# Kernel optimization log

Hardware: AMD Instinct MI355X
Metric: run time of the kernel (lower is better)

## Reference

```python
import jax, jax.numpy as jnp
import numpy as np
import math

N_HEADS = 16
HEAD_DIM = 64
D_MODEL = 1024
B, S = 2, 2048


def setup_inputs() -> dict:
    key = jax.random.key(0)
    ks = jax.random.split(key, 12)
    Dh = N_HEADS * HEAD_DIM
    sc = 1.0 / math.sqrt(D_MODEL)
    return {
        "will_be_queries": jax.random.normal(ks[0], (B, S, D_MODEL), jnp.float32),
        "will_be_keys": jax.random.normal(ks[1], (B, S, D_MODEL), jnp.float32),
        "will_be_values": jax.random.normal(ks[2], (B, S, D_MODEL), jnp.float32),
        "valid_len": jax.random.randint(ks[3], (B,), 1, S + 1, jnp.int32),
        # torch nn.Linear weights: (out_features, in_features)
        "w_q": jax.random.normal(ks[4], (Dh, D_MODEL), jnp.float32) * sc,
        "b_q": jnp.zeros((Dh,), jnp.float32),
        "w_k": jax.random.normal(ks[5], (Dh, D_MODEL), jnp.float32) * sc,
        "b_k": jnp.zeros((Dh,), jnp.float32),
        "w_v": jax.random.normal(ks[6], (Dh, D_MODEL), jnp.float32) * sc,
        "b_v": jnp.zeros((Dh,), jnp.float32),
        "w_o": jax.random.normal(ks[7], (D_MODEL, Dh), jnp.float32) * sc,
        "b_o": jnp.zeros((D_MODEL,), jnp.float32),
    }


def _split_heads(x):
    # (B, S, H*Dh) -> (B, H, S, Dh)
    b, s, _ = x.shape
    return x.reshape(b, s, N_HEADS, HEAD_DIM).transpose(0, 2, 1, 3)


def reference(will_be_queries, will_be_keys, will_be_values, valid_len,
              w_q, b_q, w_k, b_k, w_v, b_v, w_o, b_o):
    q = _split_heads(will_be_queries @ w_q.T + b_q)   # (B,H,S,Dh)
    k = _split_heads(will_be_keys @ w_k.T + b_k)
    v = _split_heads(will_be_values @ w_v.T + b_v)

    scores = jnp.einsum("bhqd,bhkd->bhqk", q, k) / jnp.sqrt(
        jnp.asarray(HEAD_DIM, q.dtype))

    neg = jnp.finfo(scores.dtype).min
    q_idx = jnp.arange(scores.shape[2])[:, None]   # (S,1)
    k_idx = jnp.arange(scores.shape[3])[None, :]   # (1,S)
    causal = k_idx > q_idx                         # look-ahead mask (offset=1 triu)
    vmask = k_idx[None] >= valid_len[:, None, None]  # (B,S,S) keys beyond valid_len
    mask = causal[None, None] | vmask[:, None]       # (B,1|H,S,S) broadcast over heads
    scores = jnp.where(mask, neg, scores)

    attn = jax.nn.softmax(scores, axis=-1)
    out = jnp.einsum("bhqk,bhkd->bhqd", attn, v)   # (B,H,S,Dh)
    out = out.transpose(0, 2, 1, 3).reshape(out.shape[0], out.shape[2], N_HEADS * HEAD_DIM)
    return out @ w_o.T + b_o
```

## Files before the change

kernel.cpp:

```cpp
#include <hip/hip_runtime.h>
#include <math.h>

#define NH 16
#define HD 64
#define DM 1024
#define BB 2
#define SS 2048
#define MROWS (BB*SS)
#define MEG 1048576

typedef __attribute__((ext_vector_type(8))) short bf16x8;
typedef __attribute__((ext_vector_type(4))) float f32x4;

__device__ __forceinline__ unsigned short f2bf(float x) {
    unsigned int u = __float_as_uint(x);
    u += 0x7fff + ((u >> 16) & 1);
    return (unsigned short)(u >> 16);
}

__device__ __forceinline__ unsigned int pack2bf(float a, float b) {
    return (unsigned int)f2bf(a) | ((unsigned int)f2bf(b) << 16);
}

#define GLD_LDS16(gp, lp) __builtin_amdgcn_global_load_lds(                  \
        (const __attribute__((address_space(1))) void*)(gp),                 \
        (__attribute__((address_space(3))) void*)(lp), 16, 0, 0)

__global__ __launch_bounds__(256)
void cvt_all(const float* __restrict__ xq, const float* __restrict__ xk,
             const float* __restrict__ xv, const float* __restrict__ wq,
             const float* __restrict__ wk, const float* __restrict__ wv,
             const float* __restrict__ wo, unsigned short* __restrict__ ws)
{
    const int reg = blockIdx.y;
    const size_t n    = (reg < 3) ? (size_t)4 * MEG : (size_t)MEG;
    const size_t roff = (reg < 3) ? (size_t)reg * 4 * MEG
                                  : (size_t)12 * MEG + (size_t)(reg - 3) * MEG;
    const float* src = (reg == 0) ? xq : (reg == 1) ? xk : (reg == 2) ? xv :
                       (reg == 3) ? wq : (reg == 4) ? wk : (reg == 5) ? wv : wo;
    const size_t i = ((size_t)blockIdx.x * 256 + threadIdx.x) * 8;
    if (i >= n) return;
    const float4 a = *(const float4*)(src + i);
    const float4 b = *(const float4*)(src + i + 4);
    ushort4 lo4, hi4;
    lo4.x = f2bf(a.x); lo4.y = f2bf(a.y); lo4.z = f2bf(a.z); lo4.w = f2bf(a.w);
    hi4.x = f2bf(b.x); hi4.y = f2bf(b.y); hi4.z = f2bf(b.z); hi4.w = f2bf(b.w);
    *(ushort4*)(ws + roff + i)     = lo4;
    *(ushort4*)(ws + roff + i + 4) = hi4;
}

template<int MODE>
__device__ __forceinline__ void gemm_mfma_core(
    const unsigned short* __restrict__ A,
    const unsigned short* __restrict__ W,
    const float* __restrict__ bias,
    void* __restrict__ Y, int ldy,
    unsigned short* __restrict__ As,
    unsigned short* __restrict__ Bs)
{
    const int tid  = threadIdx.x;
    const int w    = tid >> 6;
    const int lane = tid & 63;
    const int lo   = lane & 15;
    const int g    = lane >> 4;
    const int wr   = (w >> 1) * 64;
    const int wc   = (w & 1) * 64;

    f32x4 acc[4][4];
#pragma unroll
    for (int i = 0; i < 4; ++i)
#pragma unroll
        for (int j = 0; j < 4; ++j) acc[i][j] = (f32x4)0.f;

    for (int k0 = 0; k0 < 1024; k0 += 64) {
        __syncthreads();
#pragma unroll
        for (int u = 0; u < 4; ++u) {
            const int ci  = u * 256 + tid;
            const int row = ci >> 3, c = ci & 7;
            const int sc  = (c ^ (row & 7)) * 8;
            GLD_LDS16(A + (size_t)row * 1024 + k0 + sc, As + ci * 8);
            GLD_LDS16(W + (size_t)row * 1024 + k0 + sc, Bs + ci * 8);
        }
        asm volatile("s_waitcnt vmcnt(0)" ::: "memory");
        __syncthreads();

#pragma unroll
        for (int kk = 0; kk < 2; ++kk) {
            bf16x8 af[4], bf[4];
#pragma unroll
            for (int i = 0; i < 4; ++i) {
                const int ra = wr + i * 16 + lo;
                const int rb = wc + i * 16 + lo;
                af[i] = *(const bf16x8*)(As + ra * 64 + (((kk * 4 + g) ^ (ra & 7)) * 8));
                bf[i] = *(const bf16x8*)(Bs + rb * 64 + (((kk * 4 + g) ^ (rb & 7)) * 8));
            }
#pragma unroll
            for (int i = 0; i < 4; ++i)
#pragma unroll
                for (int j = 0; j < 4; ++j)
                    acc[i][j] = __builtin_amdgcn_mfma_f32_16x16x32_bf16(
                        af[i], bf[j], acc[i][j], 0, 0, 0);
        }
    }

#pragma unroll
    for (int i = 0; i < 4; ++i) {
#pragma unroll
        for (int j = 0; j < 4; ++j) {
            const int col = wc + j * 16 + lo;
#pragma unroll
            for (int r = 0; r < 4; ++r) {
                const int row = wr + i * 16 + g * 4 + r;
                if constexpr (MODE == 2) {
                    const float v = acc[i][j][r] + bias[row];
                    const int jc = (col & ~63) | ((((col >> 3) & 7) ^ (row & 7)) << 3)
                                 | (col & 7);
                    ((unsigned short*)Y)[(size_t)row * ldy + jc] = f2bf(v);
                } else {
                    const float v = acc[i][j][r] + bias[col];
                    if constexpr (MODE == 0)
                        ((unsigned short*)Y)[(size_t)row * ldy + col] = f2bf(v);
                    else
                        ((float*)Y)[(size_t)row * ldy + col] = v;
                }
            }
        }
    }
}

__global__ __launch_bounds__(256)
void qkv_proj(const unsigned short* __restrict__ ws,
              const float* __restrict__ bq, const float* __restrict__ bk,
              const float* __restrict__ bv,
              unsigned short* __restrict__ qk, unsigned short* __restrict__ vt)
{
    __shared__ unsigned short As[128 * 64];
    __shared__ unsigned short Bs[128 * 64];
    const int wg   = blockIdx.x;
    const int flat = (wg & 7) * 96 + (wg >> 3);
    const int fg   = flat >> 3;
    const int sub  = flat & 7;
    const int mat  = fg >> 5;
    const int r    = fg & 31;
    if (mat < 2) {
        const int m0   = r * 128;
        const int ncol = sub * 128;
        const unsigned short* A = ws + (size_t)mat * 4 * MEG + (size_t)m0 * 1024;
        const unsigned short* W = ws + (size_t)12 * MEG + (size_t)mat * MEG
                                     + (size_t)ncol * 1024;
        const float* bias = ((mat == 0) ? bq : bk) + ncol;
        gemm_mfma_core<0>(A, W, bias,
                          qk + (size_t)m0 * 2048 + mat * 1024 + ncol, 2048, As, Bs);
    } else {
        const int b      = r >> 4;
        const int colblk = r & 15;
        const int rowblk = sub;
        const unsigned short* A = ws + (size_t)14 * MEG + (size_t)rowblk * 128 * 1024;
        const unsigned short* W = ws + (size_t)8 * MEG + (size_t)b * 2 * MEG
                                     + (size_t)colblk * 128 * 1024;
        gemm_mfma_core<2>(A, W, bv + rowblk * 128,
                          vt + (size_t)b * 1024 * 2048
                             + (size_t)rowblk * 128 * 2048 + colblk * 128, 2048,
                          As, Bs);
    }
}

__global__ __launch_bounds__(256)
void out_proj(const unsigned short* __restrict__ ws,
              const float* __restrict__ bo, float* __restrict__ out)
{
    __shared__ unsigned short As[128 * 64];
    __shared__ unsigned short Bs[128 * 64];
    const int wg   = blockIdx.x;
    const int flat = (wg & 7) * 32 + (wg >> 3);
    const int m0   = (flat >> 3) * 128;
    const int n0   = (flat & 7) * 128;
    const unsigned short* A = ws + (size_t)28 * MEG + (size_t)m0 * 1024;
    const unsigned short* W = ws + (size_t)15 * MEG + (size_t)n0 * 1024;
    gemm_mfma_core<1>(A, W, bo + n0, out + (size_t)m0 * 1024 + n0, 1024, As, Bs);
}

__global__ __launch_bounds__(256)
void attn_mfma(const unsigned short* __restrict__ qk,
               const unsigned short* __restrict__ vt,
               const int* __restrict__ vlen, unsigned short* __restrict__ aout)
{
    __shared__ unsigned short Ks[2][64 * 64];
    __shared__ unsigned short Vs[2][64 * 64];
    __shared__ unsigned short Ps[4][16 * 64];

    const int bh  = blockIdx.x;
    const int qt  = 31 - blockIdx.y;
    const int b   = bh >> 4;
    const int h   = bh & 15;
    const int q0  = qt * 64;
    const int vl  = vlen[b];
    const int tid = threadIdx.x;
    const int w    = tid >> 6;
    const int lane = tid & 63;
    const int lo   = lane & 15;
    const int g    = lane >> 4;
    const int lx   = lo & 7;

    const unsigned short* qbase = qk + (size_t)(b * SS) * 2048 + h * 64;
    const unsigned short* kbase = qbase + 1024;
    const unsigned short* vtb   = vt + (size_t)b * 1024 * 2048
                                     + (size_t)(h * 64) * 2048;

    const int qg = q0 + w * 16 + lo;
    const bf16x8 a0 = *(const bf16x8*)(qbase + (size_t)qg * 2048 + g * 8);
    const bf16x8 a1 = *(const bf16x8*)(qbase + (size_t)qg * 2048 + 32 + g * 8);

    float lR = 0.f;
    f32x4 of[4];
#pragma unroll
    for (int f = 0; f < 4; ++f) of[f] = (f32x4)0.f;

    const int kmax   = min(q0 + 64, vl);
    const int ntiles = (kmax + 63) >> 6;

#pragma unroll
    for (int uu = 0; uu < 2; ++uu) {
        const int e = w * 128 + uu * 64 + lane;
        const int r = e >> 3, c = e & 7;
        GLD_LDS16(kbase + (size_t)r * 2048 + ((c ^ (r & 7)) * 8), &Ks[0][e * 8]);
        GLD_LDS16(vtb + (size_t)r * 2048 + c * 8, &Vs[0][e * 8]);
    }

    unsigned short* const Psw = Ps[w];
    const float SC = 0.125f * 1.44269504f;

    for (int kt = 0; kt < ntiles; ++kt) {
        const int cur = kt & 1;
        const int k0  = kt * 64;
        if (kt + 1 < ntiles) {
            const int kn = k0 + 64;
#pragma unroll
            for (int uu = 0; uu < 2; ++uu) {
                const int e = w * 128 + uu * 64 + lane;
                const int r = e >> 3, c = e & 7;
                GLD_LDS16(kbase + (size_t)(kn + r) * 2048 + ((c ^ (r & 7)) * 8),
                          &Ks[cur ^ 1][e * 8]);
                GLD_LDS16(vtb + (size_t)r * 2048 + kn + c * 8, &Vs[cur ^ 1][e * 8]);
            }
            asm volatile("s_waitcnt vmcnt(4)" ::: "memory");
        } else {
            asm volatile("s_waitcnt vmcnt(0)" ::: "memory");
        }
        __syncthreads();

        f32x4 sf[4];
#pragma unroll
        for (int f = 0; f < 4; ++f) sf[f] = (f32x4)0.f;
        __builtin_amdgcn_s_setprio(1);
#pragma unroll
        for (int f = 0; f < 4; ++f) {
            const int kr = f * 16 + lo;
            const bf16x8 kb0 = *(const bf16x8*)(&Ks[cur][kr * 64 + ((g ^ lx) * 8)]);
            const bf16x8 kb1 = *(const bf16x8*)(&Ks[cur][kr * 64 + (((4 + g) ^ lx) * 8)]);
            sf[f] = __builtin_amdgcn_mfma_f32_16x16x32_bf16(kb0, a0, sf[f], 0, 0, 0);
            sf[f] = __builtin_amdgcn_mfma_f32_16x16x32_bf16(kb1, a1, sf[f], 0, 0, 0);
        }
        __builtin_amdgcn_s_setprio(0);

        const bool full = (k0 + 63 <= q0 + w * 16) && (k0 + 64 <= vl);
#pragma unroll
        for (int f = 0; f < 4; ++f) {
            float p[4];
#pragma unroll
            for (int r = 0; r < 4; ++r) {
                float xv = sf[f][r];
                if (!full) {
                    const int kg = k0 + f * 16 + g * 4 + r;
                    xv = (kg <= qg && kg < vl) ? xv : -INFINITY;
                }
                p[r] = exp2f(xv * SC);
            }
            lR += (p[0] + p[1]) + (p[2] + p[3]);
            uint2 pw;
            pw.x = pack2bf(p[0], p[1]);
            pw.y = pack2bf(p[2], p[3]);
            *(uint2*)(Psw + lo * 64 + (((f * 2 + (g >> 1)) ^ lx) * 8)
                      + (g & 1) * 4) = pw;
        }

        __builtin_amdgcn_s_setprio(1);
#pragma unroll
        for (int kk = 0; kk < 2; ++kk) {
            const bf16x8 pa = *(const bf16x8*)(Psw + lo * 64
                                + (((kk * 4 + g) ^ lx) * 8));
#pragma unroll
            for (int f = 0; f < 4; ++f) {
                const bf16x8 vb = *(const bf16x8*)(&Vs[cur][(f * 16 + lo) * 64
                                    + (((4 * kk + g) ^ lx) * 8)]);
                of[f] = __builtin_amdgcn_mfma_f32_16x16x32_bf16(vb, pa, of[f], 0, 0, 0);
            }
        }
        __builtin_amdgcn_s_setprio(0);
        __syncthreads();
    }

    lR += __shfl_xor(lR, 16);
    lR += __shfl_xor(lR, 32);

    const float rv = 1.0f / lR;
    unsigned short* ob = aout + (size_t)(b * SS + q0 + w * 16 + lo) * 1024 + h * 64;
#pragma unroll
    for (int f = 0; f < 4; ++f) {
        ushort4 ov;
        ov.x = f2bf(of[f][0] * rv);
        ov.y = f2bf(of[f][1] * rv);
        ov.z = f2bf(of[f][2] * rv);
        ov.w = f2bf(of[f][3] * rv);
        *(ushort4*)(ob + f * 16 + g * 4) = ov;
    }
}

extern "C" void kernel_launch(void* const* d_in, const int* in_sizes, int n_in,
                              void* d_out, int out_size, void* d_ws, size_t ws_size,
                              hipStream_t stream) {
    const float* xq = (const float*)d_in[0];
    const float* xk = (const float*)d_in[1];
    const float* xv = (const float*)d_in[2];
    const int*   vl = (const int*)  d_in[3];
    const float* wq = (const float*)d_in[4];
    const float* bq = (const float*)d_in[5];
    const float* wk = (const float*)d_in[6];
    const float* bk = (const float*)d_in[7];
    const float* wv = (const float*)d_in[8];
    const float* bv = (const float*)d_in[9];
    const float* wo = (const float*)d_in[10];
    const float* bo = (const float*)d_in[11];

    unsigned short* ws     = (unsigned short*)d_ws;
    unsigned short* qkbuf  = ws + (size_t)16 * MEG;
    unsigned short* vtbuf  = ws + (size_t)24 * MEG;
    unsigned short* abuf   = ws + (size_t)28 * MEG;

    cvt_all<<<dim3(2048, 7), 256, 0, stream>>>(xq, xk, xv, wq, wk, wv, wo, ws);
    qkv_proj<<<dim3(768), 256, 0, stream>>>(ws, bq, bk, bv, qkbuf, vtbuf);
    attn_mfma<<<dim3(BB * NH, SS / 64), 256, 0, stream>>>(qkbuf, vtbuf, vl, abuf);
    out_proj<<<dim3(256), 256, 0, stream>>>(ws, bo, (float*)d_out);
}
```

Before: 125.4 us.

## Double attention query tile to 128 rows so each K/V tile is reused

Each attention block now handles 128 query rows instead of 64, and each wave computes two 16-row sub-tiles against every K/V tile it loads into LDS. This halves the K/V traffic and the barrier count per query row. The grid drops from 1024 to 512 blocks, with a new tile ordering meant to balance the causal workload. The software bf16 packing is also replaced by the hardware v_cvt_pk_bf16_f32 instruction. The trade-off is higher register and LDS use and fewer blocks, which could worsen causal load imbalance.

```diff
diff --git a/kernel.cpp b/kernel.cpp
--- a/kernel.cpp
+++ b/kernel.cpp
@@ -18,8 +18,10 @@
     return (unsigned short)(u >> 16);
 }
 
-__device__ __forceinline__ unsigned int pack2bf(float a, float b) {
-    return (unsigned int)f2bf(a) | ((unsigned int)f2bf(b) << 16);
+__device__ __forceinline__ unsigned int cvtpk_bf16(float a, float b) {
+    unsigned int r;
+    asm("v_cvt_pk_bf16_f32 %0, %1, %2" : "=v"(r) : "v"(a), "v"(b));
+    return r;
 }
 
 #define GLD_LDS16(gp, lp) __builtin_amdgcn_global_load_lds(                  \
@@ -188,13 +190,14 @@
 {
     __shared__ unsigned short Ks[2][64 * 64];
     __shared__ unsigned short Vs[2][64 * 64];
-    __shared__ unsigned short Ps[4][16 * 64];
+    __shared__ unsigned short Ps[4][2][16 * 64];
 
     const int bh  = blockIdx.x;
-    const int qt  = 31 - blockIdx.y;
+    const int y   = blockIdx.y;
+    const int Qt  = (y < 8) ? y : (23 - y);
     const int b   = bh >> 4;
     const int h   = bh & 15;
-    const int q0  = qt * 64;
+    const int q0  = Qt * 128;
     const int vl  = vlen[b];
     const int tid = threadIdx.x;
     const int w    = tid >> 6;
@@ -208,16 +211,22 @@
     const unsigned short* vtb   = vt + (size_t)b * 1024 * 2048
                                      + (size_t)(h * 64) * 2048;
 
-    const int qg = q0 + w * 16 + lo;
-    const bf16x8 a0 = *(const bf16x8*)(qbase + (size_t)qg * 2048 + g * 8);
-    const bf16x8 a1 = *(const bf16x8*)(qbase + (size_t)qg * 2048 + 32 + g * 8);
-
-    float lR = 0.f;
-    f32x4 of[4];
-#pragma unroll
-    for (int f = 0; f < 4; ++f) of[f] = (f32x4)0.f;
-
-    const int kmax   = min(q0 + 64, vl);
+    bf16x8 a0[2], a1[2];
+#pragma unroll
+    for (int s = 0; s < 2; ++s) {
+        const int qg = q0 + w * 32 + s * 16 + lo;
+        a0[s] = *(const bf16x8*)(qbase + (size_t)qg * 2048 + g * 8);
+        a1[s] = *(const bf16x8*)(qbase + (size_t)qg * 2048 + 32 + g * 8);
+    }
+
+    float lR[2] = {0.f, 0.f};
+    f32x4 of[2][4];
+#pragma unroll
+    for (int s = 0; s < 2; ++s)
+#pragma unroll
+        for (int f = 0; f < 4; ++f) of[s][f] = (f32x4)0.f;
+
+    const int kmax   = min(q0 + 128, vl);
     const int ntiles = (kmax + 63) >> 6;
 
 #pragma unroll
@@ -228,7 +237,6 @@
         GLD_LDS16(vtb + (size_t)r * 2048 + c * 8, &Vs[0][e * 8]);
     }
 
-    unsigned short* const Psw = Ps[w];
     const float SC = 0.125f * 1.44269504f;
 
     for (int kt = 0; kt < ntiles; ++kt) {
@@ -250,70 +258,84 @@
         }
         __syncthreads();
 
-        f32x4 sf[4];
-#pragma unroll
-        for (int f = 0; f < 4; ++f) sf[f] = (f32x4)0.f;
+        f32x4 sf[2][4];
+#pragma unroll
+        for (int s = 0; s < 2; ++s)
+#pragma unroll
+            for (int f = 0; f < 4; ++f) sf[s][f] = (f32x4)0.f;
         __builtin_amdgcn_s_setprio(1);
 #pragma unroll
         for (int f = 0; f < 4; ++f) {
             const int kr = f * 16 + lo;
             const bf16x8 kb0 = *(const bf16x8*)(&Ks[cur][kr * 64 + ((g ^ lx) * 8)]);
             const bf16x8 kb1 = *(const bf16x8*)(&Ks[cur][kr * 64 + (((4 + g) ^ lx) * 8)]);
-            sf[f] = __builtin_amdgcn_mfma_f32_16x16x32_bf16(kb0, a0, sf[f], 0, 0, 0);
-            sf[f] = __builtin_amdgcn_mfma_f32_16x16x32_bf16(kb1, a1, sf[f], 0, 0, 0);
+#pragma unroll
+            for (int s = 0; s < 2; ++s) {
+                sf[s][f] = __builtin_amdgcn_mfma_f32_16x16x32_bf16(kb0, a0[s], sf[s][f], 0, 0, 0);
+                sf[s][f] = __builtin_amdgcn_mfma_f32_16x16x32_bf16(kb1, a1[s], sf[s][f], 0, 0, 0);
+            }
         }
         __builtin_amdgcn_s_setprio(0);
 
-        const bool full = (k0 + 63 <= q0 + w * 16) && (k0 + 64 <= vl);
-#pragma unroll
-        for (int f = 0; f < 4; ++f) {
-            float p[4];
-#pragma unroll
-            for (int r = 0; r < 4; ++r) {
-                float xv = sf[f][r];
-                if (!full) {
-                    const int kg = k0 + f * 16 + g * 4 + r;
-                    xv = (kg <= qg && kg < vl) ? xv : -INFINITY;
+#pragma unroll
+        for (int s = 0; s < 2; ++s) {
+            const int qg   = q0 + w * 32 + s * 16 + lo;
+            const bool full = (k0 + 63 <= q0 + w * 32 + s * 16) && (k0 + 64 <= vl);
+#pragma unroll
+            for (int f = 0; f < 4; ++f) {
+                float p[4];
+#pragma unroll
+                for (int r = 0; r < 4; ++r) {
+                    float xv = sf[s][f][r];
+                    if (!full) {
+                        const int kg = k0 + f * 16 + g * 4 + r;
+                        xv = (kg <= qg && kg < vl) ? xv : -INFINITY;
+                    }
+                    p[r] = exp2f(xv * SC);
                 }
-                p[r] = exp2f(xv * SC);
-            }
-            lR += (p[0] + p[1]) + (p[2] + p[3]);
-            uint2 pw;
-            pw.x = pack2bf(p[0], p[1]);
-            pw.y = pack2bf(p[2], p[3]);
-            *(uint2*)(Psw + lo * 64 + (((f * 2 + (g >> 1)) ^ lx) * 8)
-                      + (g & 1) * 4) = pw;
+                lR[s] += (p[0] + p[1]) + (p[2] + p[3]);
+                uint2 pw;
+                pw.x = cvtpk_bf16(p[0], p[1]);
+                pw.y = cvtpk_bf16(p[2], p[3]);
+                *(uint2*)(&Ps[w][s][lo * 64 + (((f * 2 + (g >> 1)) ^ lx) * 8)
+                          + (g & 1) * 4]) = pw;
+            }
         }
 
         __builtin_amdgcn_s_setprio(1);
 #pragma unroll
         for (int kk = 0; kk < 2; ++kk) {
-            const bf16x8 pa = *(const bf16x8*)(Psw + lo * 64
-                                + (((kk * 4 + g) ^ lx) * 8));
+            const bf16x8 pa0 = *(const bf16x8*)(&Ps[w][0][lo * 64 + (((kk * 4 + g) ^ lx) * 8)]);
+            const bf16x8 pa1 = *(const bf16x8*)(&Ps[w][1][lo * 64 + (((kk * 4 + g) ^ lx) * 8)]);
 #pragma unroll
             for (int f = 0; f < 4; ++f) {
                 const bf16x8 vb = *(const bf16x8*)(&Vs[cur][(f * 16 + lo) * 64
                                     + (((4 * kk + g) ^ lx) * 8)]);
-                of[f] = __builtin_amdgcn_mfma_f32_16x16x32_bf16(vb, pa, of[f], 0, 0, 0);
+                of[0][f] = __builtin_amdgcn_mfma_f32_16x16x32_bf16(vb, pa0, of[0][f], 0, 0, 0);
+                of[1][f] = __builtin_amdgcn_mfma_f32_16x16x32_bf16(vb, pa1, of[1][f], 0, 0, 0);
             }
         }
         __builtin_amdgcn_s_setprio(0);
         __syncthreads();
     }
 
-    lR += __shfl_xor(lR, 16);
-    lR += __shfl_xor(lR, 32);
-
-    const float rv = 1.0f / lR;
-    unsigned short* ob = aout + (size_t)(b * SS + q0 + w * 16 + lo) * 1024 + h * 64;
-#pragma unroll
-    for (int f = 0; f < 4; ++f) {
-        ushort4 ov;
-        ov.x = f2bf(of[f][0] * rv);
-        ov.y = f2bf(of[f][1] * rv);
-        ov.z = f2bf(of[f][2] * rv);
-        ov.w = f2bf(of[f][3] * rv);
-        *(ushort4*)(ob + f * 16 + g * 4) = ov;
+#pragma unroll
+    for (int s = 0; s < 2; ++s) {
+        float l = lR[s];
+        l += __shfl_xor(l, 16);
+        l += __shfl_xor(l, 32);
+        const float rv = 1.0f / l;
+        unsigned short* ob = aout + (size_t)(b * SS + q0 + w * 32 + s * 16 + lo) * 1024
+                                  + h * 64;
+#pragma unroll
+        for (int f = 0; f < 4; ++f) {
+            ushort4 ov;
+            ov.x = f2bf(of[s][f][0] * rv);
+            ov.y = f2bf(of[s][f][1] * rv);
+            ov.z = f2bf(of[s][f][2] * rv);
+            ov.w = f2bf(of[s][f][3] * rv);
+            *(ushort4*)(ob + f * 16 + g * 4) = ov;
+        }
     }
 }
 
@@ -340,6 +362,6 @@
 
     cvt_all<<<dim3(2048, 7), 256, 0, stream>>>(xq, xk, xv, wq, wk, wv, wo, ws);
     qkv_proj<<<dim3(768), 256, 0, stream>>>(ws, bq, bk, bv, qkbuf, vtbuf);
-    attn_mfma<<<dim3(BB * NH, SS / 64), 256, 0, stream>>>(qkbuf, vtbuf, vl, abuf);
+    attn_mfma<<<dim3(BB * NH, 16), 256, 0, stream>>>(qkbuf, vtbuf, vl, abuf);
     out_proj<<<dim3(256), 256, 0, stream>>>(ws, bo, (float*)d_out);
 }
```

After: 143.6 us. 14.6% more time.

## Fuse fp32-to-bf16 activation conversion into QKV projection tile loads

Applied to the files above, without the earlier changes.

The separate conversion pass now handles only the weight matrices. The QKV projection GEMM reads the fp32 query, key and value activations directly, converts each tile to bf16 in registers and writes it to LDS. This removes a full write and re-read of 12M bf16 activation elements through global memory. In exchange the activation tile loads become synchronous register loads plus LDS stores instead of async global-to-LDS copies, and each tile is re-read as fp32 by every column block, so the GEMM moves more global bytes.

```diff
diff --git a/kernel.cpp b/kernel.cpp
--- a/kernel.cpp
+++ b/kernel.cpp
@@ -27,37 +27,36 @@
         (__attribute__((address_space(3))) void*)(lp), 16, 0, 0)
 
 __global__ __launch_bounds__(256)
-void cvt_all(const float* __restrict__ xq, const float* __restrict__ xk,
-             const float* __restrict__ xv, const float* __restrict__ wq,
-             const float* __restrict__ wk, const float* __restrict__ wv,
-             const float* __restrict__ wo, unsigned short* __restrict__ ws)
-{
-    const int reg = blockIdx.y;
-    const size_t n    = (reg < 3) ? (size_t)4 * MEG : (size_t)MEG;
-    const size_t roff = (reg < 3) ? (size_t)reg * 4 * MEG
-                                  : (size_t)12 * MEG + (size_t)(reg - 3) * MEG;
-    const float* src = (reg == 0) ? xq : (reg == 1) ? xk : (reg == 2) ? xv :
-                       (reg == 3) ? wq : (reg == 4) ? wk : (reg == 5) ? wv : wo;
+void cvt_w(const float* __restrict__ wq, const float* __restrict__ wk,
+           const float* __restrict__ wv, const float* __restrict__ wo,
+           unsigned short* __restrict__ ws)
+{
+    const int m = blockIdx.y;
+    const float* src = (m == 0) ? wq : (m == 1) ? wk : (m == 2) ? wv : wo;
     const size_t i = ((size_t)blockIdx.x * 256 + threadIdx.x) * 8;
-    if (i >= n) return;
     const float4 a = *(const float4*)(src + i);
     const float4 b = *(const float4*)(src + i + 4);
     ushort4 lo4, hi4;
     lo4.x = f2bf(a.x); lo4.y = f2bf(a.y); lo4.z = f2bf(a.z); lo4.w = f2bf(a.w);
     hi4.x = f2bf(b.x); hi4.y = f2bf(b.y); hi4.z = f2bf(b.z); hi4.w = f2bf(b.w);
-    *(ushort4*)(ws + roff + i)     = lo4;
-    *(ushort4*)(ws + roff + i + 4) = hi4;
-}
-
-template<int MODE>
+    unsigned short* dst = ws + (size_t)12 * MEG + (size_t)m * MEG + i;
+    *(ushort4*)(dst)     = lo4;
+    *(ushort4*)(dst + 4) = hi4;
+}
+
+template<int MODE, bool AF32, bool WF32>
 __device__ __forceinline__ void gemm_mfma_core(
-    const unsigned short* __restrict__ A,
-    const unsigned short* __restrict__ W,
+    const void* __restrict__ A_, const void* __restrict__ W_,
     const float* __restrict__ bias,
     void* __restrict__ Y, int ldy,
     unsigned short* __restrict__ As,
     unsigned short* __restrict__ Bs)
 {
+    const unsigned short* Ab = (const unsigned short*)A_;
+    const float*          Af = (const float*)A_;
+    const unsigned short* Wb = (const unsigned short*)W_;
+    const float*          Wf = (const float*)W_;
+
     const int tid  = threadIdx.x;
     const int w    = tid >> 6;
     const int lane = tid & 63;
@@ -79,8 +78,52 @@
             const int ci  = u * 256 + tid;
             const int row = ci >> 3, c = ci & 7;
             const int sc  = (c ^ (row & 7)) * 8;
-            GLD_LDS16(A + (size_t)row * 1024 + k0 + sc, As + ci * 8);
-            GLD_LDS16(W + (size_t)row * 1024 + k0 + sc, Bs + ci * 8);
+            if constexpr (!AF32)
+                GLD_LDS16(Ab + (size_t)row * 1024 + k0 + sc, As + ci * 8);
+            if constexpr (!WF32)
+                GLD_LDS16(Wb + (size_t)row * 1024 + k0 + sc, Bs + ci * 8);
+        }
+        if constexpr (AF32) {
+            float4 f[4][2];
+#pragma unroll
+            for (int u = 0; u < 4; ++u) {
+                const int ci = u * 256 + tid, row = ci >> 3, c = ci & 7;
+                const int sc = (c ^ (row & 7)) * 8;
+                const float* s = Af + (size_t)row * 1024 + k0 + sc;
+                f[u][0] = *(const float4*)s;
+                f[u][1] = *(const float4*)(s + 4);
+            }
+#pragma unroll
+            for (int u = 0; u < 4; ++u) {
+                const int ci = u * 256 + tid;
+                uint4 pw;
+                pw.x = pack2bf(f[u][0].x, f[u][0].y);
+                pw.y = pack2bf(f[u][0].z, f[u][0].w);
+                pw.z = pack2bf(f[u][1].x, f[u][1].y);
+                pw.w = pack2bf(f[u][1].z, f[u][1].w);
+                *(uint4*)(As + ci * 8) = pw;
+            }
+        }
+        if constexpr (WF32) {
+            float4 f[4][2];
+#pragma unroll
+            for (int u = 0; u < 4; ++u) {
+                const int ci = u * 256 + tid, row = ci >> 3, c = ci & 7;
+                const int sc = (c ^ (row & 7)) * 8;
+                const float* s = Wf + (size_t)row * 1024 + k0 + sc;
+                f[u][0] = *(const float4*)s;
+                f[u][1] = *(const float4*)(s + 4);
+            }
+#pragma unroll
+            for (int u = 0; u < 4; ++u) {
+                const int ci = u * 256 + tid;
+                uint4 pw;
+                pw.x = pack2bf(f[u][0].x, f[u][0].y);
+                pw.y = pack2bf(f[u][0].z, f[u][0].w);
+                pw.z = pack2bf(f[u][1].x, f[u][1].y);
+                pw.w = pack2bf(f[u][1].z, f[u][1].w);
+                *(uint4*)(Bs + ci * 8) = pw;
+            }
         }
         asm volatile("s_waitcnt vmcnt(0)" ::: "memory");
         __syncthreads();
@@ -130,7 +173,8 @@
 }
 
 __global__ __launch_bounds__(256)
-void qkv_proj(const unsigned short* __restrict__ ws,
+void qkv_proj(const float* __restrict__ xq, const float* __restrict__ xk,
+              const float* __restrict__ xv, const unsigned short* __restrict__ ws,
               const float* __restrict__ bq, const float* __restrict__ bk,
               const float* __restrict__ bv,
               unsigned short* __restrict__ qk, unsigned short* __restrict__ vt)
@@ -146,20 +190,19 @@
     if (mat < 2) {
         const int m0   = r * 128;
         const int ncol = sub * 128;
-        const unsigned short* A = ws + (size_t)mat * 4 * MEG + (size_t)m0 * 1024;
+        const float* A = ((mat == 0) ? xq : xk) + (size_t)m0 * 1024;
         const unsigned short* W = ws + (size_t)12 * MEG + (size_t)mat * MEG
                                      + (size_t)ncol * 1024;
         const float* bias = ((mat == 0) ? bq : bk) + ncol;
-        gemm_mfma_core<0>(A, W, bias,
+        gemm_mfma_core<0, true, false>(A, W, bias,
                           qk + (size_t)m0 * 2048 + mat * 1024 + ncol, 2048, As, Bs);
     } else {
         const int b      = r >> 4;
         const int colblk = r & 15;
         const int rowblk = sub;
         const unsigned short* A = ws + (size_t)14 * MEG + (size_t)rowblk * 128 * 1024;
-        const unsigned short* W = ws + (size_t)8 * MEG + (size_t)b * 2 * MEG
-                                     + (size_t)colblk * 128 * 1024;
-        gemm_mfma_core<2>(A, W, bv + rowblk * 128,
+        const float* W = xv + (size_t)b * 2 * MEG + (size_t)colblk * 128 * 1024;
+        gemm_mfma_core<2, false, true>(A, W, bv + rowblk * 128,
                           vt + (size_t)b * 1024 * 2048
                              + (size_t)rowblk * 128 * 2048 + colblk * 128, 2048,
                           As, Bs);
@@ -178,7 +221,8 @@
     const int n0   = (flat & 7) * 128;
     const unsigned short* A = ws + (size_t)28 * MEG + (size_t)m0 * 1024;
     const unsigned short* W = ws + (size_t)15 * MEG + (size_t)n0 * 1024;
-    gemm_mfma_core<1>(A, W, bo + n0, out + (size_t)m0 * 1024 + n0, 1024, As, Bs);
+    gemm_mfma_core<1, false, false>(A, W, bo + n0,
+                                    out + (size_t)m0 * 1024 + n0, 1024, As, Bs);
 }
 
 __global__ __launch_bounds__(256)
@@ -338,8 +382,9 @@
     unsigned short* vtbuf  = ws + (size_t)24 * MEG;
     unsigned short* abuf   = ws + (size_t)28 * MEG;
 
-    cvt_all<<<dim3(2048, 7), 256, 0, stream>>>(xq, xk, xv, wq, wk, wv, wo, ws);
-    qkv_proj<<<dim3(768), 256, 0, stream>>>(ws, bq, bk, bv, qkbuf, vtbuf);
+    cvt_w<<<dim3(512, 4), 256, 0, stream>>>(wq, wk, wv, wo, ws);
+    qkv_proj<<<dim3(768), 256, 0, stream>>>(xq, xk, xv, ws, bq, bk, bv,
+                                            qkbuf, vtbuf);
     attn_mfma<<<dim3(BB * NH, SS / 64), 256, 0, stream>>>(qkbuf, vtbuf, vl, abuf);
     out_proj<<<dim3(256), 256, 0, stream>>>(ws, bo, (float*)d_out);
 }
```

Result: slower. 130.5 us (+4.1%).

## Prefetch attention K/V tiles through registers into single LDS buffer; reorder query tiles

Applied to the files above, without the earlier changes.

Replaces the double-buffered direct global-to-LDS loads of K and V tiles with register prefetch. Each step loads the next tile into registers while computing the current one, then writes it to a single LDS buffer after a barrier. This halves K/V shared memory, which may raise occupancy, but adds an extra barrier per step and costs more VGPRs. Query tiles are also remapped from a strict reverse order to a zig-zag order across blockIdx.y, changing how causal work is balanced across workgroups.

```diff
diff --git a/kernel.cpp b/kernel.cpp
--- a/kernel.cpp
+++ b/kernel.cpp
@@ -186,12 +186,15 @@
                const unsigned short* __restrict__ vt,
                const int* __restrict__ vlen, unsigned short* __restrict__ aout)
 {
-    __shared__ unsigned short Ks[2][64 * 64];
-    __shared__ unsigned short Vs[2][64 * 64];
+    __shared__ unsigned short Ks[64 * 64];
+    __shared__ unsigned short Vs[64 * 64];
     __shared__ unsigned short Ps[4][16 * 64];
 
     const int bh  = blockIdx.x;
-    const int qt  = 31 - blockIdx.y;
+    const int y   = blockIdx.y;
+    const int yq  = y & 7, yt = y >> 3;
+    const int qt  = (yt == 0) ? yq : (yt == 1) ? (15 - yq)
+                  : (yt == 2) ? (16 + yq) : (31 - yq);
     const int b   = bh >> 4;
     const int h   = bh & 15;
     const int q0  = qt * 64;
@@ -220,35 +223,44 @@
     const int kmax   = min(q0 + 64, vl);
     const int ntiles = (kmax + 63) >> 6;
 
+    int ee[2], er[2], ec[2];
 #pragma unroll
     for (int uu = 0; uu < 2; ++uu) {
-        const int e = w * 128 + uu * 64 + lane;
-        const int r = e >> 3, c = e & 7;
-        GLD_LDS16(kbase + (size_t)r * 2048 + ((c ^ (r & 7)) * 8), &Ks[0][e * 8]);
-        GLD_LDS16(vtb + (size_t)r * 2048 + c * 8, &Vs[0][e * 8]);
-    }
+        ee[uu] = w * 128 + uu * 64 + lane;
+        er[uu] = ee[uu] >> 3;
+        ec[uu] = ee[uu] & 7;
+    }
+
+    uint4 kreg[2], vreg[2];
+#pragma unroll
+    for (int uu = 0; uu < 2; ++uu) {
+        kreg[uu] = *(const uint4*)(kbase + (size_t)er[uu] * 2048
+                                   + ((ec[uu] ^ (er[uu] & 7)) * 8));
+        vreg[uu] = *(const uint4*)(vtb + (size_t)er[uu] * 2048 + ec[uu] * 8);
+    }
+#pragma unroll
+    for (int uu = 0; uu < 2; ++uu) {
+        *(uint4*)&Ks[ee[uu] * 8] = kreg[uu];
+        *(uint4*)&Vs[ee[uu] * 8] = vreg[uu];
+    }
+    __syncthreads();
 
     unsigned short* const Psw = Ps[w];
     const float SC = 0.125f * 1.44269504f;
 
     for (int kt = 0; kt < ntiles; ++kt) {
-        const int cur = kt & 1;
-        const int k0  = kt * 64;
-        if (kt + 1 < ntiles) {
+        const int k0   = kt * 64;
+        const bool more = (kt + 1 < ntiles);
+        if (more) {
             const int kn = k0 + 64;
 #pragma unroll
             for (int uu = 0; uu < 2; ++uu) {
-                const int e = w * 128 + uu * 64 + lane;
-                const int r = e >> 3, c = e & 7;
-                GLD_LDS16(kbase + (size_t)(kn + r) * 2048 + ((c ^ (r & 7)) * 8),
-                          &Ks[cur ^ 1][e * 8]);
-                GLD_LDS16(vtb + (size_t)r * 2048 + kn + c * 8, &Vs[cur ^ 1][e * 8]);
-            }
-            asm volatile("s_waitcnt vmcnt(4)" ::: "memory");
-        } else {
-            asm volatile("s_waitcnt vmcnt(0)" ::: "memory");
-        }
-        __syncthreads();
+                kreg[uu] = *(const uint4*)(kbase + (size_t)(kn + er[uu]) * 2048
+                                           + ((ec[uu] ^ (er[uu] & 7)) * 8));
+                vreg[uu] = *(const uint4*)(vtb + (size_t)er[uu] * 2048 + kn
+                                           + ec[uu] * 8);
+            }
+        }
 
         f32x4 sf[4];
 #pragma unroll
@@ -257,8 +269,8 @@
 #pragma unroll
         for (int f = 0; f < 4; ++f) {
             const int kr = f * 16 + lo;
-            const bf16x8 kb0 = *(const bf16x8*)(&Ks[cur][kr * 64 + ((g ^ lx) * 8)]);
-            const bf16x8 kb1 = *(const bf16x8*)(&Ks[cur][kr * 64 + (((4 + g) ^ lx) * 8)]);
+            const bf16x8 kb0 = *(const bf16x8*)(&Ks[kr * 64 + ((g ^ lx) * 8)]);
+            const bf16x8 kb1 = *(const bf16x8*)(&Ks[kr * 64 + (((4 + g) ^ lx) * 8)]);
             sf[f] = __builtin_amdgcn_mfma_f32_16x16x32_bf16(kb0, a0, sf[f], 0, 0, 0);
             sf[f] = __builtin_amdgcn_mfma_f32_16x16x32_bf16(kb1, a1, sf[f], 0, 0, 0);
         }
@@ -292,20 +304,29 @@
                                 + (((kk * 4 + g) ^ lx) * 8));
 #pragma unroll
             for (int f = 0; f < 4; ++f) {
-                const bf16x8 vb = *(const bf16x8*)(&Vs[cur][(f * 16 + lo) * 64
+                const bf16x8 vb = *(const bf16x8*)(&Vs[(f * 16 + lo) * 64
                                     + (((4 * kk + g) ^ lx) * 8)]);
                 of[f] = __builtin_amdgcn_mfma_f32_16x16x32_bf16(vb, pa, of[f], 0, 0, 0);
             }
         }
         __builtin_amdgcn_s_setprio(0);
+
         __syncthreads();
+        if (more) {
+#pragma unroll
+            for (int uu = 0; uu < 2; ++uu) {
+                *(uint4*)&Ks[ee[uu] * 8] = kreg[uu];
+                *(uint4*)&Vs[ee[uu] * 8] = vreg[uu];
+            }
+            __syncthreads();
+        }
     }
 
     lR += __shfl_xor(lR, 16);
     lR += __shfl_xor(lR, 32);
 
     const float rv = 1.0f / lR;
-    unsigned short* ob = aout + (size_t)(b * SS + q0 + w * 16 + lo) * 1024 + h * 64;
+    unsigned short* ob = aout + (size_t)(b * SS + qg) * 1024 + h * 64;
 #pragma unroll
     for (int f = 0; f < 4; ++f) {
         ushort4 ov;
```

Result: slower. 170.4 us (+36.0%).
